# Kernel optimization log

Measured on AMD Instinct MI355X. Metric: run time of the kernel, lower is better.

Reference implementation:

```python
import jax, jax.numpy as jnp
import numpy as np

N_NODES = 50000
N_EDGES = 800000
D_IN = 128
D_OUT = 128


def setup_inputs() -> dict:
    key = jax.random.key(0)
    k1, k2, k3, k4 = jax.random.split(key, 4)
    X = jax.random.normal(k1, (N_NODES, D_IN), dtype=jnp.float32)
    weight = jax.random.normal(k2, (D_IN, D_OUT), dtype=jnp.float32) * (1.0 / np.sqrt(D_OUT))
    edge_src = jax.random.randint(k3, (N_EDGES,), 0, N_NODES, dtype=jnp.int32)
    edge_dst = jax.random.randint(k4, (N_EDGES,), 0, N_NODES, dtype=jnp.int32)
    return {"X": X, "weight": weight, "edge_src": edge_src, "edge_dst": edge_dst}


def reference(X, weight, edge_src, edge_dst):
    # GCN: out = A_hat_hat @ (X @ W), A_hat_hat = D^-1/2 (A + I) D^-1/2
    ones = jnp.ones((edge_src.shape[0],), dtype=X.dtype)
    # node degrees (+1 for implicit self loop, avoids div-by-zero)
    deg = jax.ops.segment_sum(ones, edge_dst, num_segments=N_NODES) + 1.0
    inv_sqrt_deg = jax.lax.rsqrt(deg)  # [N]
    XW = X @ weight  # [N, D_OUT] dense GEMM
    # per-edge normalization 1/sqrt(d_i * d_j)
    norm = inv_sqrt_deg[edge_dst] * inv_sqrt_deg[edge_src]  # [E]
    msg = XW[edge_src] * norm[:, None]  # [E, D_OUT] gather
    agg = jax.ops.segment_sum(msg, edge_dst, num_segments=N_NODES)  # scatter-add
    # self-loop contribution: 1/d_i * XW[i]
    out = agg + XW * (inv_sqrt_deg * inv_sqrt_deg)[:, None]
    return out
```

## Files before the change

### kernel.cpp

```cpp
#include <hip/hip_runtime.h>

#define N_NODES 50000
#define N_EDGES 800000
#define D 128

#define NBLK 250
#define EPB (N_EDGES / NBLK)
#define NQ (EPB / 4)
#define NBKT 196
#define CAP 6144

typedef __attribute__((ext_vector_type(8))) short bf16x8;
typedef __attribute__((ext_vector_type(4))) float f32x4;

static const size_t OFF_TOT  = 0;
static const size_t OFF_WT   = 1024;
static const size_t OFF_H    = 33792;
static const size_t OFF_BB   = 234496;
static const size_t OFF_DEG  = 435200;
static const size_t OFF_OFFS = 635200;
static const size_t OFF_IVS  = 835200;
static const size_t OFF_REC  = 1235200;
static const size_t OFF_CSR  = 6052096;
static const size_t OFF_XWQ  = 8460544;

#define BM 64
#define NB_GEMM ((N_NODES + BM - 1) / BM)

__device__ __forceinline__ unsigned short f2bf(float f) {
    unsigned int u = __float_as_uint(f);
    unsigned int r = (u + 0x7fffu + ((u >> 16) & 1u)) >> 16;
    return (unsigned short)r;
}
__device__ __forceinline__ float sb(unsigned int u, int i) {
    return (float)((int)(u << (24 - 8 * i)) >> 24);
}

__global__ __launch_bounds__(256) void k_pre(const int* __restrict__ dst,
                                             int* __restrict__ H,
                                             const float* __restrict__ W,
                                             unsigned short* __restrict__ Wt) {
    __shared__ unsigned int cnt[256];
    int bid = blockIdx.x, t = threadIdx.x;
    if (bid >= NBLK) {
        int idx = (bid - NBLK) * 256 + t;
        int n = idx >> 7, k = idx & 127;
        Wt[n * D + k] = f2bf(W[k * D + n]);
        return;
    }
    cnt[t] = 0;
    __syncthreads();
    int e0 = bid * EPB;
    for (int q = t; q < NQ; q += 256) {
        int4 d4 = *(const int4*)&dst[e0 + q * 4];
        atomicAdd(&cnt[d4.x >> 8], 1u);
        atomicAdd(&cnt[d4.y >> 8], 1u);
        atomicAdd(&cnt[d4.z >> 8], 1u);
        atomicAdd(&cnt[d4.w >> 8], 1u);
    }
    __syncthreads();
    if (t < NBKT) H[t * 256 + bid] = (int)cnt[t];
}

__global__ __launch_bounds__(256) void k_pB(const int* __restrict__ H,
                                            int* __restrict__ BB,
                                            int* __restrict__ TOT) {
    int k = blockIdx.x, t = threadIdx.x;
    int w = t >> 6, l = t & 63;
    int v = (t < NBLK) ? H[k * 256 + t] : 0;
    int s = v;
    #pragma unroll
    for (int d = 1; d < 64; d <<= 1) {
        int u = __shfl_up(s, d, 64);
        if (l >= d) s += u;
    }
    __shared__ int wtot[4], woff[4];
    if (l == 63) wtot[w] = s;
    __syncthreads();
    if (t == 0) {
        woff[0] = 0; woff[1] = wtot[0];
        woff[2] = wtot[0] + wtot[1]; woff[3] = wtot[0] + wtot[1] + wtot[2];
    }
    __syncthreads();
    int excl = s - v + woff[w];
    BB[k * 256 + t] = excl;
    if (t == 255) TOT[k] = excl + v;
}

__global__ __launch_bounds__(512) void k_pC(const int* __restrict__ src,
                                            const int* __restrict__ dst,
                                            const int* __restrict__ BB,
                                            unsigned int* __restrict__ rec) {
    __shared__ unsigned int cnt[200];
    __shared__ int myBB[NBKT];
    int b = blockIdx.x, t = threadIdx.x;
    if (t < 200) cnt[t] = 0;
    if (t < NBKT) myBB[t] = t * CAP + BB[t * 256 + b];
    __syncthreads();
    int e0 = b * EPB;
    for (int q = t; q < NQ; q += 512) {
        int4 d4 = *(const int4*)&dst[e0 + q * 4];
        int4 s4 = *(const int4*)&src[e0 + q * 4];
        {
            int k = d4.x >> 8;
            unsigned int r = atomicAdd(&cnt[k], 1u);
            rec[myBB[k] + (int)r] = (unsigned int)s4.x | ((unsigned int)(d4.x & 255) << 16);
        }
        {
            int k = d4.y >> 8;
            unsigned int r = atomicAdd(&cnt[k], 1u);
            rec[myBB[k] + (int)r] = (unsigned int)s4.y | ((unsigned int)(d4.y & 255) << 16);
        }
        {
            int k = d4.z >> 8;
            unsigned int r = atomicAdd(&cnt[k], 1u);
            rec[myBB[k] + (int)r] = (unsigned int)s4.z | ((unsigned int)(d4.z & 255) << 16);
        }
        {
            int k = d4.w >> 8;
            unsigned int r = atomicAdd(&cnt[k], 1u);
            rec[myBB[k] + (int)r] = (unsigned int)s4.w | ((unsigned int)(d4.w & 255) << 16);
        }
    }
}

__global__ __launch_bounds__(256) void k_mid(const unsigned int* __restrict__ rec,
                                             const int* __restrict__ TOT,
                                             int* __restrict__ deg,
                                             int* __restrict__ offs,
                                             float* __restrict__ ivs,
                                             unsigned short* __restrict__ csr,
                                             const float* __restrict__ X,
                                             const unsigned short* __restrict__ Wt,
                                             char* __restrict__ XWq) {
    __shared__ unsigned short sB[D * D];
    __shared__ int wtot[4], woff[4];
    int bid = blockIdx.x;
    int t = threadIdx.x;
    int w = t >> 6, l = t & 63;

    if (bid >= NBKT) {
        int r0 = (bid - NBKT) * BM;

        #pragma unroll
        for (int p = 0; p < 8; ++p) {
            int e = p * 2048 + t * 8;
            int n = e >> 7, k = e & 127;
            uint4 v = *(const uint4*)&Wt[e];
            int idx = n * D + (((k >> 3) ^ (n & 7)) << 3);
            *(uint4*)&sB[idx] = v;
        }
        __syncthreads();

        int arow = w * 16 + (l & 15);
        int xrow = r0 + arow;
        bool okr = (xrow < N_NODES);
        f32x4 acc[8];
        #pragma unroll
        for (int i = 0; i < 8; ++i) acc[i] = (f32x4){0.f, 0.f, 0.f, 0.f};

        #pragma unroll
        for (int kk = 0; kk < 4; ++kk) {
            int g = kk * 4 + (l >> 4);
            float4 xa = make_float4(0.f, 0.f, 0.f, 0.f);
            float4 xb = make_float4(0.f, 0.f, 0.f, 0.f);
            if (okr) {
                xa = *(const float4*)&X[xrow * D + g * 8];
                xb = *(const float4*)&X[xrow * D + g * 8 + 4];
            }
            bf16x8 a;
            a[0] = (short)f2bf(xa.x); a[1] = (short)f2bf(xa.y);
            a[2] = (short)f2bf(xa.z); a[3] = (short)f2bf(xa.w);
            a[4] = (short)f2bf(xb.x); a[5] = (short)f2bf(xb.y);
            a[6] = (short)f2bf(xb.z); a[7] = (short)f2bf(xb.w);
            #pragma unroll
            for (int nt = 0; nt < 8; ++nt) {
                int nrow = nt * 16 + (l & 15);
                bf16x8 b = *(bf16x8*)&sB[nrow * D + ((g ^ (nrow & 7)) << 3)];
                acc[nt] = __builtin_amdgcn_mfma_f32_16x16x32_bf16(a, b, acc[nt], 0, 0, 0);
            }
        }

        float rmax[4];
        #pragma unroll
        for (int r = 0; r < 4; ++r) {
            float m = 0.f;
            #pragma unroll
            for (int nt = 0; nt < 8; ++nt) m = fmaxf(m, fabsf(acc[nt][r]));
            #pragma unroll
            for (int d = 1; d < 16; d <<= 1) m = fmaxf(m, __shfl_xor(m, d, 64));
            rmax[r] = fmaxf(m, 1e-20f);
        }

        #pragma unroll
        for (int r = 0; r < 4; ++r) {
            float qs = 127.0f / rmax[r];
            int row = w * 16 + (l >> 4) * 4 + r;
            int m = r0 + row;
            if (m < N_NODES) {
                char q8[8];
                #pragma unroll
                for (int nt = 0; nt < 8; ++nt) {
                    float f = acc[nt][r] * qs;
                    f = fminf(fmaxf(f, -127.0f), 127.0f);
                    q8[nt] = (char)__float2int_rn(f);
                }
                #pragma unroll
                for (int nt = 0; nt < 8; ++nt)
                    XWq[(size_t)m * D + nt * 16 + (l & 15)] = q8[nt];
                if ((l & 15) == 0) ivs[m * 2 + 1] = rmax[r] * (1.0f / 127.0f);
            }
        }
        return;
    }

    unsigned int* lcnt = (unsigned int*)sB;
    int* off_l = ((int*)sB) + 256;
    int k = bid;
    int base = k * CAP;
    int tot = TOT[k];

    lcnt[t] = 0;
    __syncthreads();
    for (int i = t; i < tot; i += 256)
        atomicAdd(&lcnt[rec[base + i] >> 16], 1u);
    __syncthreads();

    int v = (int)lcnt[t];
    int vr = (v + 3) & ~3;
    int s = vr;
    #pragma unroll
    for (int d = 1; d < 64; d <<= 1) {
        int u = __shfl_up(s, d, 64);
        if (l >= d) s += u;
    }
    if (l == 63) wtot[w] = s;
    __syncthreads();
    if (t == 0) {
        woff[0] = 0; woff[1] = wtot[0];
        woff[2] = wtot[0] + wtot[1]; woff[3] = wtot[0] + wtot[1] + wtot[2];
    }
    __syncthreads();
    int excl = s - vr + woff[w];
    off_l[t] = excl;
    int node = k * 256 + t;
    if (node < N_NODES) {
        deg[node] = v;
        ivs[node * 2] = rsqrtf((float)v + 1.0f);
        offs[node] = base + excl;
    }
    for (int j = v; j < vr; ++j) csr[base + excl + j] = 0;
    __syncthreads();
    lcnt[t] = 0;
    __syncthreads();
    for (int i = t; i < tot; i += 256) {
        unsigned int rc = rec[base + i];
        int dl = rc >> 16;
        unsigned int r = atomicAdd(&lcnt[dl], 1u);
        csr[base + off_l[dl] + (int)r] = (unsigned short)(rc & 0xFFFFu);
    }
}

__global__ __launch_bounds__(256) void k_agg(const char* __restrict__ XWq,
                                             const float2* __restrict__ ivs,
                                             const unsigned short* __restrict__ csr,
                                             const int* __restrict__ offs,
                                             const int* __restrict__ deg,
                                             float* __restrict__ out) {
    __shared__ int s_off[16];
    __shared__ int s_cnt[16];
    __shared__ float2 s_iv[16];
    int n0 = blockIdx.x * 16;
    int t = threadIdx.x;
    if (t < 16) {
        int n = n0 + t;
        int ok = (n < N_NODES);
        s_off[t] = ok ? offs[n] : 0;
        s_cnt[t] = ok ? deg[n] : -1;
        s_iv[t] = ok ? ivs[n] : make_float2(0.f, 0.f);
    }
    __syncthreads();
    int li = t >> 4;
    int cl = t & 15;
    int node = n0 + li;
    int cnt = s_cnt[li];
    if (cnt < 0) return;
    int start = s_off[li];
    float2 vs = s_iv[li];
    float invd = vs.x;

    float acc[8];
    {
        float sc = invd * invd * vs.y;
        uint2 v = *(const uint2*)&XWq[(size_t)node * D + cl * 8];
        acc[0] = sc * sb(v.x, 0); acc[1] = sc * sb(v.x, 1);
        acc[2] = sc * sb(v.x, 2); acc[3] = sc * sb(v.x, 3);
        acc[4] = sc * sb(v.y, 0); acc[5] = sc * sb(v.y, 1);
        acc[6] = sc * sb(v.y, 2); acc[7] = sc * sb(v.y, 3);
    }

    for (int e = 0; e < cnt; e += 8) {
        uint2 ca = *(const uint2*)&csr[start + e];
        uint2 cb = *(const uint2*)&csr[start + e + 4];
        int si[8];
        si[0] = ca.x & 0xffff; si[1] = ca.x >> 16;
        si[2] = ca.y & 0xffff; si[3] = ca.y >> 16;
        si[4] = cb.x & 0xffff; si[5] = cb.x >> 16;
        si[6] = cb.y & 0xffff; si[7] = cb.y >> 16;
        uint2 v[8];
        float nn[8];
        #pragma unroll
        for (int u = 0; u < 8; ++u) {
            v[u] = *(const uint2*)&XWq[(size_t)si[u] * D + cl * 8];
            float2 iv = ivs[si[u]];
            nn[u] = (e + u < cnt) ? invd * iv.x * iv.y : 0.f;
        }
        #pragma unroll
        for (int u = 0; u < 8; ++u) {
            float n = nn[u];
            acc[0] += n * sb(v[u].x, 0); acc[1] += n * sb(v[u].x, 1);
            acc[2] += n * sb(v[u].x, 2); acc[3] += n * sb(v[u].x, 3);
            acc[4] += n * sb(v[u].y, 0); acc[5] += n * sb(v[u].y, 1);
            acc[6] += n * sb(v[u].y, 2); acc[7] += n * sb(v[u].y, 3);
        }
    }

    f32x4 o0 = (f32x4){acc[0], acc[1], acc[2], acc[3]};
    f32x4 o1 = (f32x4){acc[4], acc[5], acc[6], acc[7]};
    __builtin_nontemporal_store(o0, (f32x4*)&out[node * D + cl * 8]);
    __builtin_nontemporal_store(o1, (f32x4*)&out[node * D + cl * 8 + 4]);
}

extern "C" void kernel_launch(void* const* d_in, const int* in_sizes, int n_in,
                              void* d_out, int out_size, void* d_ws, size_t ws_size,
                              hipStream_t stream) {
    const float* X = (const float*)d_in[0];
    const float* W = (const float*)d_in[1];
    const int* esrc = (const int*)d_in[2];
    const int* edst = (const int*)d_in[3];
    float* out = (float*)d_out;

    char* ws = (char*)d_ws;
    int* TOT = (int*)(ws + OFF_TOT);
    unsigned short* Wt = (unsigned short*)(ws + OFF_WT);
    int* H = (int*)(ws + OFF_H);
    int* BB = (int*)(ws + OFF_BB);
    int* deg = (int*)(ws + OFF_DEG);
    int* offs = (int*)(ws + OFF_OFFS);
    float* ivs = (float*)(ws + OFF_IVS);
    unsigned int* rec = (unsigned int*)(ws + OFF_REC);
    unsigned short* csr = (unsigned short*)(ws + OFF_CSR);
    char* XWq = (char*)(ws + OFF_XWQ);

    k_pre<<<NBLK + 64, 256, 0, stream>>>(edst, H, W, Wt);
    k_pB<<<NBKT, 256, 0, stream>>>(H, BB, TOT);
    k_pC<<<NBLK, 512, 0, stream>>>(esrc, edst, BB, rec);
    k_mid<<<NBKT + NB_GEMM, 256, 0, stream>>>(rec, TOT, deg, offs, ivs, csr,
                                              X, Wt, XWq);
    k_agg<<<(N_NODES + 15) / 16, 256, 0, stream>>>(XWq, (const float2*)ivs, csr,
                                                   offs, deg, out);
}
```

Before: 61.62 us.

## Assign one wavefront per node and split edges across four lane groups

The aggregation kernel now gives each node a full 64-lane wavefront instead of 16 lanes. Four 16-lane groups each take every fourth edge, and the partial sums are combined with cross-lane shuffles before lanes 0-15 write the output row. This raises the number of gathers in flight per node and removes the shared-memory staging and block barrier. The cost is four times as many threads, extra shuffle work, and idle lanes on low-degree nodes. The csr padding now has to cover 16-edge chunks, which the preprocessing kernel may not guarantee.

```diff
diff --git a/kernel.cpp b/kernel.cpp
--- a/kernel.cpp
+++ b/kernel.cpp
@@ -267,30 +267,21 @@
                                              const int* __restrict__ offs,
                                              const int* __restrict__ deg,
                                              float* __restrict__ out) {
-    __shared__ int s_off[16];
-    __shared__ int s_cnt[16];
-    __shared__ float2 s_iv[16];
-    int n0 = blockIdx.x * 16;
-    int t = threadIdx.x;
-    if (t < 16) {
-        int n = n0 + t;
-        int ok = (n < N_NODES);
-        s_off[t] = ok ? offs[n] : 0;
-        s_cnt[t] = ok ? deg[n] : -1;
-        s_iv[t] = ok ? ivs[n] : make_float2(0.f, 0.f);
-    }
-    __syncthreads();
-    int li = t >> 4;
-    int cl = t & 15;
-    int node = n0 + li;
-    int cnt = s_cnt[li];
-    if (cnt < 0) return;
-    int start = s_off[li];
-    float2 vs = s_iv[li];
+    int node = (blockIdx.x * 256 + threadIdx.x) >> 6;
+    if (node >= N_NODES) return;
+    int l = threadIdx.x & 63;
+    int eg = l >> 4;
+    int cl = l & 15;
+
+    int start = offs[node];
+    int cnt = deg[node];
+    float2 vs = ivs[node];
     float invd = vs.x;
 
     float acc[8];
-    {
+    #pragma unroll
+    for (int j = 0; j < 8; ++j) acc[j] = 0.f;
+    if (eg == 0) {
         float sc = invd * invd * vs.y;
         uint2 v = *(const uint2*)&XWq[(size_t)node * D + cl * 8];
         acc[0] = sc * sb(v.x, 0); acc[1] = sc * sb(v.x, 1);
@@ -299,24 +290,32 @@
         acc[6] = sc * sb(v.y, 2); acc[7] = sc * sb(v.y, 3);
     }
 
-    for (int e = 0; e < cnt; e += 8) {
-        uint2 ca = *(const uint2*)&csr[start + e];
-        uint2 cb = *(const uint2*)&csr[start + e + 4];
-        int si[8];
-        si[0] = ca.x & 0xffff; si[1] = ca.x >> 16;
-        si[2] = ca.y & 0xffff; si[3] = ca.y >> 16;
-        si[4] = cb.x & 0xffff; si[5] = cb.x >> 16;
-        si[6] = cb.y & 0xffff; si[7] = cb.y >> 16;
-        uint2 v[8];
-        float nn[8];
-        #pragma unroll
-        for (int u = 0; u < 8; ++u) {
+    for (int e = 0; e < cnt; e += 16) {
+        uint2 q0 = *(const uint2*)&csr[start + e];
+        uint2 q1 = *(const uint2*)&csr[start + e + 4];
+        uint2 q2 = *(const uint2*)&csr[start + e + 8];
+        uint2 q3 = *(const uint2*)&csr[start + e + 12];
+        int si[4];
+        {
+            unsigned int h0 = (eg & 2) ? q0.y : q0.x;
+            unsigned int h1 = (eg & 2) ? q1.y : q1.x;
+            unsigned int h2 = (eg & 2) ? q2.y : q2.x;
+            unsigned int h3 = (eg & 2) ? q3.y : q3.x;
+            si[0] = (eg & 1) ? (h0 >> 16) : (h0 & 0xffff);
+            si[1] = (eg & 1) ? (h1 >> 16) : (h1 & 0xffff);
+            si[2] = (eg & 1) ? (h2 >> 16) : (h2 & 0xffff);
+            si[3] = (eg & 1) ? (h3 >> 16) : (h3 & 0xffff);
+        }
+        uint2 v[4];
+        float nn[4];
+        #pragma unroll
+        for (int u = 0; u < 4; ++u) {
             v[u] = *(const uint2*)&XWq[(size_t)si[u] * D + cl * 8];
             float2 iv = ivs[si[u]];
-            nn[u] = (e + u < cnt) ? invd * iv.x * iv.y : 0.f;
-        }
-        #pragma unroll
-        for (int u = 0; u < 8; ++u) {
+            nn[u] = (e + u * 4 + eg < cnt) ? invd * iv.x * iv.y : 0.f;
+        }
+        #pragma unroll
+        for (int u = 0; u < 4; ++u) {
             float n = nn[u];
             acc[0] += n * sb(v[u].x, 0); acc[1] += n * sb(v[u].x, 1);
             acc[2] += n * sb(v[u].x, 2); acc[3] += n * sb(v[u].x, 3);
@@ -325,10 +324,18 @@
         }
     }
 
-    f32x4 o0 = (f32x4){acc[0], acc[1], acc[2], acc[3]};
-    f32x4 o1 = (f32x4){acc[4], acc[5], acc[6], acc[7]};
-    __builtin_nontemporal_store(o0, (f32x4*)&out[node * D + cl * 8]);
-    __builtin_nontemporal_store(o1, (f32x4*)&out[node * D + cl * 8 + 4]);
+    #pragma unroll
+    for (int j = 0; j < 8; ++j) {
+        acc[j] += __shfl_xor(acc[j], 16, 64);
+        acc[j] += __shfl_xor(acc[j], 32, 64);
+    }
+
+    if (l < 16) {
+        f32x4 o0 = (f32x4){acc[0], acc[1], acc[2], acc[3]};
+        f32x4 o1 = (f32x4){acc[4], acc[5], acc[6], acc[7]};
+        __builtin_nontemporal_store(o0, (f32x4*)&out[node * D + cl * 8]);
+        __builtin_nontemporal_store(o1, (f32x4*)&out[node * D + cl * 8 + 4]);
+    }
 }
 
 extern "C" void kernel_launch(void* const* d_in, const int* in_sizes, int n_in,
@@ -357,6 +364,6 @@
     k_pC<<<NBLK, 512, 0, stream>>>(esrc, edst, BB, rec);
     k_mid<<<NBKT + NB_GEMM, 256, 0, stream>>>(rec, TOT, deg, offs, ivs, csr,
                                               X, Wt, XWq);
-    k_agg<<<(N_NODES + 15) / 16, 256, 0, stream>>>(XWq, (const float2*)ivs, csr,
-                                                   offs, deg, out);
-}
+    k_agg<<<(N_NODES * 64 + 255) / 256, 256, 0, stream>>>(XWq, (const float2*)ivs,
+                                                          csr, offs, deg, out);
+}
```

Measured after the change: 65.01 us. 1.06x slower.
